# Performance work log

Measured on AMD Instinct MI355X. Metric: run time of the kernel, lower is better.

Reference implementation:

```python
import jax, jax.numpy as jnp
import numpy as np

GROUP_SIZE = 128


def _dequant_groupwise(values, scales, group_size):
    # values: [rows, cols] int codes; scales: [rows, cols//group_size]
    rows, cols = values.shape
    groups = cols // group_size  # dims chosen to divide evenly (no padding branch)
    v = values.astype(jnp.float32).reshape(rows, groups, group_size)
    return (v * scales[:, :, None]).reshape(rows, cols)


def setup_inputs() -> dict:
    key = jax.random.key(0)
    ks = jax.random.split(key, 8)
    tokens, d_in, d_out, rank = 8192, 4096, 4096, 256
    return {
        "x": jax.random.normal(ks[0], (tokens, d_in), dtype=jnp.float32),
        "q_values": jax.random.randint(ks[1], (d_out, d_in), 0, 16, dtype=jnp.int32),
        "q_scales": jax.random.uniform(ks[2], (d_out, d_in // GROUP_SIZE), dtype=jnp.float32),
        "l_values": jax.random.randint(ks[3], (d_out, rank), 0, 16, dtype=jnp.int32),
        "l_scales": jax.random.uniform(ks[4], (d_out, rank // GROUP_SIZE), dtype=jnp.float32),
        "r_values": jax.random.randint(ks[5], (rank, d_in), 0, 16, dtype=jnp.int32),
        "r_scales": jax.random.uniform(ks[6], (rank, d_in // GROUP_SIZE), dtype=jnp.float32),
        "bias": jax.random.normal(ks[7], (d_out,), dtype=jnp.float32),
    }


def reference(x, q_values, q_scales, l_values, l_scales, r_values, r_scales, bias):
    # Dequantize groupwise int-quantized weights, then y = x @ Q^T + (x @ R^T) @ L^T + b
    q = _dequant_groupwise(q_values, q_scales, GROUP_SIZE)  # [out, in]
    l = _dequant_groupwise(l_values, l_scales, GROUP_SIZE)  # [out, rank]
    r = _dequant_groupwise(r_values, r_scales, GROUP_SIZE)  # [rank, in]
    xr = jnp.einsum('ti,ri->tr', x, r)          # [tokens, rank]
    base = jnp.einsum('ti,oi->to', x, q)        # [tokens, out]
    low_rank = jnp.einsum('tr,or->to', xr, l)   # [tokens, out]
    return base + low_rank + bias
```

## Files before the change

kernel.cpp:

```cpp
#include <hip/hip_runtime.h>
#include <cstdint>
#include <cstddef>

#define BM 128
#define BN 128
#define BK 64

typedef float f32x4 __attribute__((ext_vector_type(4)));
typedef __bf16 bf16x8 __attribute__((ext_vector_type(8)));

__device__ __forceinline__ unsigned short f2bf(float f) {
    unsigned int u = __float_as_uint(f);
    u += 0x7fffu + ((u >> 16) & 1u);
    return (unsigned short)(u >> 16);
}

__device__ __forceinline__ void async_copy16(const void* g, void* l) {
    __builtin_amdgcn_global_load_lds(
        (__attribute__((address_space(1))) void*)(g),
        (__attribute__((address_space(3))) void*)(l), 16, 0, 0);
}


__global__ void cast_x_kernel(const float* __restrict__ x,
                              unsigned short* __restrict__ o, int n8) {
    int i = blockIdx.x * blockDim.x + threadIdx.x;
    if (i >= n8) return;
    const float4* xv = (const float4*)x;
    float4 a = xv[2 * (size_t)i];
    float4 b = xv[2 * (size_t)i + 1];
    union { unsigned short u[8]; uint4 v; } r;
    r.u[0] = f2bf(a.x); r.u[1] = f2bf(a.y); r.u[2] = f2bf(a.z); r.u[3] = f2bf(a.w);
    r.u[4] = f2bf(b.x); r.u[5] = f2bf(b.y); r.u[6] = f2bf(b.z); r.u[7] = f2bf(b.w);
    ((uint4*)o)[i] = r.v;
}

__global__ void dequant_kernel(const int* __restrict__ v,
                               const float* __restrict__ s,
                               unsigned short* __restrict__ o,
                               int colshift, int gpr, int n8) {
    int i = blockIdx.x * blockDim.x + threadIdx.x;
    if (i >= n8) return;
    int e = i * 8;
    int row = e >> colshift;
    int col = e & ((1 << colshift) - 1);
    float sc = s[row * gpr + (col >> 7)];
    int4 a = ((const int4*)v)[2 * (size_t)i];
    int4 b = ((const int4*)v)[2 * (size_t)i + 1];
    union { unsigned short u[8]; uint4 x; } r;
    r.u[0] = f2bf(a.x * sc); r.u[1] = f2bf(a.y * sc);
    r.u[2] = f2bf(a.z * sc); r.u[3] = f2bf(a.w * sc);
    r.u[4] = f2bf(b.x * sc); r.u[5] = f2bf(b.y * sc);
    r.u[6] = f2bf(b.z * sc); r.u[7] = f2bf(b.w * sc);
    ((uint4*)o)[i] = r.x;
}

__global__ void __launch_bounds__(256)
gemm_bt_kernel(const __bf16* __restrict__ A1, int lda1, int k1steps,
               const __bf16* __restrict__ B1,
               const __bf16* __restrict__ A2, int lda2, int k2steps,
               const __bf16* __restrict__ B2,
               const float* __restrict__ bias,
               float* __restrict__ outf,
               unsigned short* __restrict__ outb,
               int ldo) {
    __shared__ __bf16 As[BM * BK];
    __shared__ __bf16 Bs[BN * BK];

    const int tid  = threadIdx.x;
    const int lane = tid & 63;
    const int wave = tid >> 6;
    const int wm = (wave >> 1) * 64;
    const int wn = (wave & 1) * 64;
    const int mBase = blockIdx.y * BM;
    const int nBase = blockIdx.x * BN;
    const int lrow = lane >> 3;
    const int lcol = (((lane & 7) ^ lrow) & 7) * 8;

    f32x4 acc[4][4] = {};

    #pragma unroll 1
    for (int phase = 0; phase < 2; ++phase) {
        const __bf16* A = phase ? A2 : A1;
        const __bf16* B = phase ? B2 : B1;
        const int lda    = phase ? lda2 : lda1;
        const int ksteps = phase ? k2steps : k1steps;

        for (int kt = 0; kt < ksteps; ++kt) {
            const int k0 = kt * BK;
            #pragma unroll
            for (int r = 0; r < 4; ++r) {
                const int chunk = wave * 4 + r;
                const int row = chunk * 8 + lrow;
                async_copy16(A + (size_t)(mBase + row) * lda + (k0 + lcol),
                             &As[chunk * 512]);
                async_copy16(B + (size_t)(nBase + row) * lda + (k0 + lcol),
                             &Bs[chunk * 512]);
            }
            __syncthreads();

            #pragma unroll
            for (int ks = 0; ks < 2; ++ks) {
                const int kofs = ks * 32 + (lane >> 4) * 8;
                const int swz = kofs >> 3;
                bf16x8 af[4], bfr[4];
                #pragma unroll
                for (int i = 0; i < 4; ++i) {
                    const int m = wm + i * 16 + (lane & 15);
                    af[i] = *(const bf16x8*)&As[m * BK + (((swz ^ m) & 7) << 3)];
                }
                #pragma unroll
                for (int j = 0; j < 4; ++j) {
                    const int n = wn + j * 16 + (lane & 15);
                    bfr[j] = *(const bf16x8*)&Bs[n * BK + (((swz ^ n) & 7) << 3)];
                }
                #pragma unroll
                for (int i = 0; i < 4; ++i)
                    #pragma unroll
                    for (int j = 0; j < 4; ++j)
                        acc[i][j] = __builtin_amdgcn_mfma_f32_16x16x32_bf16(
                            af[i], bfr[j], acc[i][j], 0, 0, 0);
            }
            __syncthreads();
        }
    }

    const int cn = lane & 15;
    const int rg = (lane >> 4) * 4;
    if (outf) {
        #pragma unroll
        for (int j = 0; j < 4; ++j) {
            const int o = nBase + wn + j * 16 + cn;
            const float bv = bias[o];
            #pragma unroll
            for (int i = 0; i < 4; ++i) {
                const int t0 = mBase + wm + i * 16 + rg;
                #pragma unroll
                for (int r = 0; r < 4; ++r)
                    outf[(size_t)(t0 + r) * ldo + o] = acc[i][j][r] + bv;
            }
        }
    } else {
        #pragma unroll
        for (int j = 0; j < 4; ++j) {
            const int o = nBase + wn + j * 16 + cn;
            #pragma unroll
            for (int i = 0; i < 4; ++i) {
                const int t0 = mBase + wm + i * 16 + rg;
                #pragma unroll
                for (int r = 0; r < 4; ++r)
                    outb[(size_t)(t0 + r) * ldo + o] = f2bf(acc[i][j][r]);
            }
        }
    }
}

extern "C" void kernel_launch(void* const* d_in, const int* in_sizes, int n_in,
                              void* d_out, int out_size, void* d_ws, size_t ws_size,
                              hipStream_t stream) {
    const float* x    = (const float*)d_in[0];
    const int*   qv   = (const int*)d_in[1];
    const float* qs   = (const float*)d_in[2];
    const int*   lv   = (const int*)d_in[3];
    const float* ls   = (const float*)d_in[4];
    const int*   rv   = (const int*)d_in[5];
    const float* rs   = (const float*)d_in[6];
    const float* bias = (const float*)d_in[7];
    float* out = (float*)d_out;

    const int T = 8192, DI = 4096, DO = 4096, R = 256;

    char* ws = (char*)d_ws;
    unsigned short* xb = (unsigned short*)(ws);
    unsigned short* Qd = (unsigned short*)(ws + 67108864);
    unsigned short* Rd = (unsigned short*)(ws + 100663296);
    unsigned short* Ld = (unsigned short*)(ws + 102760448);
    unsigned short* xr = (unsigned short*)(ws + 104857600);

    {
        int n8 = T * DI / 8;
        cast_x_kernel<<<(n8 + 255) / 256, 256, 0, stream>>>(x, xb, n8);
    }
    {
        int n8 = DO * DI / 8;
        dequant_kernel<<<(n8 + 255) / 256, 256, 0, stream>>>(qv, qs, Qd, 12, DI / 128, n8);
    }
    {
        int n8 = DO * R / 8;
        dequant_kernel<<<(n8 + 255) / 256, 256, 0, stream>>>(lv, ls, Ld, 8, R / 128, n8);
    }
    {
        int n8 = R * DI / 8;
        dequant_kernel<<<(n8 + 255) / 256, 256, 0, stream>>>(rv, rs, Rd, 12, DI / 128, n8);
    }
    {
        dim3 g(R / BN, T / BM);
        gemm_bt_kernel<<<g, 256, 0, stream>>>(
            (const __bf16*)xb, DI, DI / BK, (const __bf16*)Rd,
            nullptr, 0, 0, nullptr,
            nullptr, nullptr, xr, R);
    }
    {
        dim3 g(DO / BN, T / BM);
        gemm_bt_kernel<<<g, 256, 0, stream>>>(
            (const __bf16*)xb, DI, DI / BK, (const __bf16*)Qd,
            (const __bf16*)xr, R, R / BK, (const __bf16*)Ld,
            bias, out, nullptr, DO);
    }
}
```

Measured before the change: 648.2 us.

## Replace main GEMM with 256x256 tile, 8-wave, double-buffered pipelined kernel

Swaps the main x@Q^T + xr@L^T GEMM from a 128x128, 4-wave, single-buffered kernel to a 256x256, 8-wave kernel. The new kernel double-buffers LDS, interleaves async global-to-LDS copies with MFMA quads, and raises MFMA priority with s_setprio. Block IDs are remapped to group tiles for L2 locality. This aims to hide memory latency behind compute and raise operand reuse, at the cost of 128KB of LDS per block, much higher register pressure, and fewer total blocks.

```diff
diff --git a/kernel.cpp b/kernel.cpp
--- a/kernel.cpp
+++ b/kernel.cpp
@@ -155,6 +155,228 @@
     }
 }
 
+
+#define SM_OFF(slot_, mat_, half_) ((((slot_) * 2 + (mat_)) * 2 + (half_)) * 8192)
+
+#define MFMA_QUAD(MG, NG, AA, BB)                                           \
+    _Pragma("unroll")                                                       \
+    for (int m_ = 0; m_ < 4; ++m_)                                          \
+        _Pragma("unroll")                                                   \
+        for (int n_ = 0; n_ < 2; ++n_)                                      \
+            _Pragma("unroll")                                               \
+            for (int k_ = 0; k_ < 2; ++k_)                                  \
+                acc[(MG)*4 + m_][(NG)*2 + n_] =                             \
+                    __builtin_amdgcn_mfma_f32_16x16x32_bf16(                \
+                        AA[m_][k_], BB[n_][k_],                             \
+                        acc[(MG)*4 + m_][(NG)*2 + n_], 0, 0, 0)
+
+__device__ __forceinline__ void run_pipeline(
+    const __bf16* __restrict__ A, const __bf16* __restrict__ B,
+    const int lda, const int nt,
+    const int mBase, const int nBase,
+    const int wave, const int lane, const int wr, const int wc,
+    __bf16* smp, f32x4 (&acc)[8][4])
+{
+    const int lrow  = lane >> 3;
+    const int lcol  = (((lane & 7) ^ lrow) & 7) * 8;
+    const int soff0 = (wave * 8 + lrow) * lda + lcol;
+    const int soff1 = ((wave + 8) * 8 + lrow) * lda + lcol;
+
+    const __bf16* Abase = A + (size_t)mBase * lda;
+    const __bf16* Bbase = B + (size_t)nBase * lda;
+
+    const int aoff0 = (lane & 15) * 64 + ((((lane >> 4))     ^ (lane & 7)) * 8);
+    const int aoff1 = (lane & 15) * 64 + (((4 + (lane >> 4)) ^ (lane & 7)) * 8);
+
+    const __bf16* Ah0 = smp + SM_OFF(0, 0, wr);
+    const __bf16* Ah1 = smp + SM_OFF(1, 0, wr);
+    const __bf16* Bh0 = smp + SM_OFF(0, 1, wc >> 1) + (wc & 1) * 4096;
+    const __bf16* Bh1 = smp + SM_OFF(1, 1, wc >> 1) + (wc & 1) * 4096;
+
+#define STAGE(base_, half_, tile_, slot_, mat_) do {                         \
+        const __bf16* g_ = (base_) + (size_t)((half_) * 128) * lda +         \
+                           (size_t)(tile_) * 64;                             \
+        __bf16* d_ = smp + SM_OFF(slot_, mat_, half_);                       \
+        async_copy16(g_ + soff0, d_ + wave * 512);                           \
+        async_copy16(g_ + soff1, d_ + (wave + 8) * 512);                     \
+    } while (0)
+
+    STAGE(Bbase, 0, 0, 0, 1);
+    STAGE(Bbase, 1, 0, 0, 1);
+    STAGE(Abase, 0, 0, 0, 0);
+    STAGE(Abase, 1, 0, 0, 0);
+    STAGE(Bbase, 0, 1, 1, 1);
+    STAGE(Bbase, 1, 1, 1, 1);
+    STAGE(Abase, 0, 1, 1, 0);
+    asm volatile("s_waitcnt vmcnt(6)" ::: "memory");
+    __builtin_amdgcn_s_barrier();
+
+    bf16x8 aR[4][2], bLo[2][2], bHi[2][2];
+
+    const int niter = nt >> 1;
+    #pragma unroll 1
+    for (int i = 0; i < niter; ++i) {
+        const int t1 = 2 * i + 1;
+        int p2 = 2 * i + 2; if (p2 >= nt) p2 = nt - 2;
+        int p3 = 2 * i + 3; if (p3 >= nt) p3 = nt - 1;
+
+        #pragma unroll
+        for (int m = 0; m < 4; ++m) {
+            aR[m][0] = *(const bf16x8*)(Ah0 + m * 1024 + aoff0);
+            aR[m][1] = *(const bf16x8*)(Ah0 + m * 1024 + aoff1);
+        }
+        #pragma unroll
+        for (int n = 0; n < 2; ++n) {
+            bLo[n][0] = *(const bf16x8*)(Bh0 + n * 1024 + aoff0);
+            bLo[n][1] = *(const bf16x8*)(Bh0 + n * 1024 + aoff1);
+        }
+        STAGE(Abase, 1, t1, 1, 0);
+        __builtin_amdgcn_s_barrier();
+        asm volatile("s_waitcnt lgkmcnt(0)" ::: "memory");
+        __builtin_amdgcn_s_setprio(1);
+        MFMA_QUAD(0, 0, aR, bLo);
+        __builtin_amdgcn_s_setprio(0);
+        __builtin_amdgcn_s_barrier();
+
+        #pragma unroll
+        for (int n = 0; n < 2; ++n) {
+            bHi[n][0] = *(const bf16x8*)(Bh0 + (2 + n) * 1024 + aoff0);
+            bHi[n][1] = *(const bf16x8*)(Bh0 + (2 + n) * 1024 + aoff1);
+        }
+        STAGE(Bbase, 0, p2, 0, 1);
+        __builtin_amdgcn_s_barrier();
+        asm volatile("s_waitcnt lgkmcnt(0)" ::: "memory");
+        __builtin_amdgcn_s_setprio(1);
+        MFMA_QUAD(0, 1, aR, bHi);
+        __builtin_amdgcn_s_setprio(0);
+        __builtin_amdgcn_s_barrier();
+
+        #pragma unroll
+        for (int m = 0; m < 4; ++m) {
+            aR[m][0] = *(const bf16x8*)(Ah0 + (4 + m) * 1024 + aoff0);
+            aR[m][1] = *(const bf16x8*)(Ah0 + (4 + m) * 1024 + aoff1);
+        }
+        STAGE(Bbase, 1, p2, 0, 1);
+        __builtin_amdgcn_s_barrier();
+        asm volatile("s_waitcnt lgkmcnt(0)" ::: "memory");
+        __builtin_amdgcn_s_setprio(1);
+        MFMA_QUAD(1, 1, aR, bHi);
+        __builtin_amdgcn_s_setprio(0);
+        __builtin_amdgcn_s_barrier();
+
+        STAGE(Abase, 0, p2, 0, 0);
+        asm volatile("s_waitcnt vmcnt(6)" ::: "memory");
+        __builtin_amdgcn_s_barrier();
+        __builtin_amdgcn_s_setprio(1);
+        MFMA_QUAD(1, 0, aR, bLo);
+        __builtin_amdgcn_s_setprio(0);
+        __builtin_amdgcn_s_barrier();
+
+        #pragma unroll
+        for (int m = 0; m < 4; ++m) {
+            aR[m][0] = *(const bf16x8*)(Ah1 + m * 1024 + aoff0);
+            aR[m][1] = *(const bf16x8*)(Ah1 + m * 1024 + aoff1);
+        }
+        #pragma unroll
+        for (int n = 0; n < 2; ++n) {
+            bLo[n][0] = *(const bf16x8*)(Bh1 + n * 1024 + aoff0);
+            bLo[n][1] = *(const bf16x8*)(Bh1 + n * 1024 + aoff1);
+        }
+        STAGE(Abase, 1, p2, 0, 0);
+        __builtin_amdgcn_s_barrier();
+        asm volatile("s_waitcnt lgkmcnt(0)" ::: "memory");
+        __builtin_amdgcn_s_setprio(1);
+        MFMA_QUAD(0, 0, aR, bLo);
+        __builtin_amdgcn_s_setprio(0);
+        __builtin_amdgcn_s_barrier();
+
+        #pragma unroll
+        for (int n = 0; n < 2; ++n) {
+            bHi[n][0] = *(const bf16x8*)(Bh1 + (2 + n) * 1024 + aoff0);
+            bHi[n][1] = *(const bf16x8*)(Bh1 + (2 + n) * 1024 + aoff1);
+        }
+        STAGE(Bbase, 0, p3, 1, 1);
+        __builtin_amdgcn_s_barrier();
+        asm volatile("s_waitcnt lgkmcnt(0)" ::: "memory");
+        __builtin_amdgcn_s_setprio(1);
+        MFMA_QUAD(0, 1, aR, bHi);
+        __builtin_amdgcn_s_setprio(0);
+        __builtin_amdgcn_s_barrier();
+
+        #pragma unroll
+        for (int m = 0; m < 4; ++m) {
+            aR[m][0] = *(const bf16x8*)(Ah1 + (4 + m) * 1024 + aoff0);
+            aR[m][1] = *(const bf16x8*)(Ah1 + (4 + m) * 1024 + aoff1);
+        }
+        STAGE(Bbase, 1, p3, 1, 1);
+        __builtin_amdgcn_s_barrier();
+        asm volatile("s_waitcnt lgkmcnt(0)" ::: "memory");
+        __builtin_amdgcn_s_setprio(1);
+        MFMA_QUAD(1, 1, aR, bHi);
+        __builtin_amdgcn_s_setprio(0);
+        __builtin_amdgcn_s_barrier();
+
+        STAGE(Abase, 0, p3, 1, 0);
+        asm volatile("s_waitcnt vmcnt(6)" ::: "memory");
+        __builtin_amdgcn_s_barrier();
+        __builtin_amdgcn_s_setprio(1);
+        MFMA_QUAD(1, 0, aR, bLo);
+        __builtin_amdgcn_s_setprio(0);
+        __builtin_amdgcn_s_barrier();
+    }
+
+    asm volatile("s_waitcnt vmcnt(0)" ::: "memory");
+    __builtin_amdgcn_s_barrier();
+#undef STAGE
+}
+
+__global__ void __launch_bounds__(512, 2)
+gemm256_kernel(const __bf16* __restrict__ A1, const __bf16* __restrict__ B1,
+               int lda1, int nt1,
+               const __bf16* __restrict__ A2, const __bf16* __restrict__ B2,
+               int lda2, int nt2,
+               const float* __restrict__ bias, float* __restrict__ out,
+               int ldo, int gxlog2) {
+    __shared__ __bf16 sm[2][2][2][8192];
+
+    const int tid  = threadIdx.x;
+    const int lane = tid & 63;
+    const int wave = tid >> 6;
+    const int wr = wave >> 2;
+    const int wc = wave & 3;
+
+    const int bid = blockIdx.x;
+    const int cpx = gridDim.x >> 3;
+    const int s   = (bid & 7) * cpx + (bid >> 3);
+    const int bx  = s & ((1 << gxlog2) - 1);
+    const int by  = s >> gxlog2;
+    const int mBase = by * 256;
+    const int nBase = bx * 256;
+
+    f32x4 acc[8][4] = {};
+
+    __bf16* smp = &sm[0][0][0][0];
+    run_pipeline(A1, B1, lda1, nt1, mBase, nBase, wave, lane, wr, wc, smp, acc);
+    run_pipeline(A2, B2, lda2, nt2, mBase, nBase, wave, lane, wr, wc, smp, acc);
+
+    const int cn = lane & 15;
+    const int rg = (lane >> 4) * 4;
+    const int row0 = mBase + wr * 128 + rg;
+    const int col0 = nBase + wc * 64 + cn;
+    #pragma unroll
+    for (int nf = 0; nf < 4; ++nf) {
+        const int o = col0 + nf * 16;
+        const float bv = bias[o];
+        #pragma unroll
+        for (int mf = 0; mf < 8; ++mf) {
+            const int t0 = row0 + mf * 16;
+            #pragma unroll
+            for (int r = 0; r < 4; ++r)
+                out[(size_t)(t0 + r) * ldo + o] = acc[mf][nf][r] + bv;
+        }
+    }
+}
+
 extern "C" void kernel_launch(void* const* d_in, const int* in_sizes, int n_in,
                               void* d_out, int out_size, void* d_ws, size_t ws_size,
                               hipStream_t stream) {
@@ -201,10 +423,10 @@
             nullptr, nullptr, xr, R);
     }
     {
-        dim3 g(DO / BN, T / BM);
-        gemm_bt_kernel<<<g, 256, 0, stream>>>(
-            (const __bf16*)xb, DI, DI / BK, (const __bf16*)Qd,
-            (const __bf16*)xr, R, R / BK, (const __bf16*)Ld,
-            bias, out, nullptr, DO);
-    }
-}
+        int nblocks = (DO / 256) * (T / 256);
+        gemm256_kernel<<<nblocks, 512, 0, stream>>>(
+            (const __bf16*)xb, (const __bf16*)Qd, DI, DI / 64,
+            (const __bf16*)xr, (const __bf16*)Ld, R, R / 64,
+            bias, out, DO, 4 );
+    }
+}
```

Measured after the change: 603.3 us. 1.07x faster.
